# Optimization experiments

Measured on AMD Instinct MI355X. Metric: run time of the kernel, lower is better.

Reference implementation:

```python
import jax, jax.numpy as jnp
import numpy as np

D_MODEL = 1024
NUM_HEADS = 16
HEAD_DIM = D_MODEL // NUM_HEADS
CAUSAL = True


def rope_cos_sin(seq_len, dim):
    inv_freq = 1.0 / (10000.0 ** (jnp.arange(0, dim, 2, dtype=jnp.float32) / dim))
    t = jnp.arange(seq_len, dtype=jnp.float32)
    freqs = jnp.einsum('i,j->ij', t, inv_freq)          # [S, dim/2]
    emb = jnp.concatenate([freqs, freqs], axis=-1)      # [S, dim]
    return jnp.cos(emb), jnp.sin(emb)


def rotate_half(x):
    x1, x2 = jnp.split(x, 2, axis=-1)
    return jnp.concatenate([-x2, x1], axis=-1)


def setup_inputs() -> dict:
    key = jax.random.key(0)
    k1, k2, k3, k4, k5 = jax.random.split(key, 5)
    B, S = 2, 2048
    x = jax.random.normal(k1, (B, S, D_MODEL), dtype=jnp.float32)
    s = 1.0 / np.sqrt(D_MODEL)
    W_qkv = jax.random.normal(k2, (D_MODEL, 3 * D_MODEL), dtype=jnp.float32) * s
    b_qkv = jax.random.normal(k3, (3 * D_MODEL,), dtype=jnp.float32) * 0.01
    W_out = jax.random.normal(k4, (D_MODEL, D_MODEL), dtype=jnp.float32) * s
    b_out = jax.random.normal(k5, (D_MODEL,), dtype=jnp.float32) * 0.01
    return {"x": x, "W_qkv": W_qkv, "b_qkv": b_qkv, "W_out": W_out, "b_out": b_out}


def reference(x, W_qkv, b_qkv, W_out, b_out):
    B, S, _ = x.shape
    qkv = x @ W_qkv + b_qkv                              # [B, S, 3D]
    q, k, v = jnp.split(qkv, 3, axis=-1)
    # [B, H, S, hd]
    q = q.reshape(B, S, NUM_HEADS, HEAD_DIM).transpose(0, 2, 1, 3)
    k = k.reshape(B, S, NUM_HEADS, HEAD_DIM).transpose(0, 2, 1, 3)
    v = v.reshape(B, S, NUM_HEADS, HEAD_DIM).transpose(0, 2, 1, 3)
    cos, sin = rope_cos_sin(S, HEAD_DIM)                 # [S, hd]
    cos = cos[None, None]
    sin = sin[None, None]
    q = q * cos + rotate_half(q) * sin
    k = k * cos + rotate_half(k) * sin
    scores = jnp.einsum('bhqd,bhkd->bhqk', q, k) / np.sqrt(HEAD_DIM)
    if CAUSAL:
        causal_mask = jnp.triu(jnp.ones((S, S), dtype=bool), k=1)
        scores = jnp.where(causal_mask, -jnp.inf, scores)
    attn = jax.nn.softmax(scores, axis=-1)
    out = jnp.einsum('bhqk,bhkd->bhqd', attn, v)         # [B, H, S, hd]
    out = out.transpose(0, 2, 1, 3).reshape(B, S, D_MODEL)
    return out @ W_out + b_out
```

## Files before the change

### kernel.cpp

```cpp
#include <hip/hip_runtime.h>
#include <hip/hip_bf16.h>
#include <math.h>

typedef __bf16 bf16;
typedef __bf16 bf16x8 __attribute__((ext_vector_type(8)));
typedef unsigned short ushort8 __attribute__((ext_vector_type(8)));
typedef float floatx4 __attribute__((ext_vector_type(4)));

#define MFMA_BF16(a, b, c) __builtin_amdgcn_mfma_f32_16x16x32_bf16(a, b, c, 0, 0, 0)

__device__ __forceinline__ bf16x8 cvt8(const float4 a, const float4 b) {
  bf16x8 t;
  t[0] = (bf16)a.x; t[1] = (bf16)a.y; t[2] = (bf16)a.z; t[3] = (bf16)a.w;
  t[4] = (bf16)b.x; t[5] = (bf16)b.y; t[6] = (bf16)b.z; t[7] = (bf16)b.w;
  return t;
}

__device__ __forceinline__ unsigned int pack2(float a, float b) {
  unsigned short lo = __builtin_bit_cast(unsigned short, (bf16)a);
  unsigned short hi = __builtin_bit_cast(unsigned short, (bf16)b);
  return (unsigned int)lo | ((unsigned int)hi << 16);
}

__device__ __forceinline__ void gld16(const bf16* g, bf16* l) {
  __builtin_amdgcn_global_load_lds(
      (const __attribute__((address_space(1))) unsigned int*)g,
      (__attribute__((address_space(3))) unsigned int*)l, 16, 0, 0);
}

__global__ __launch_bounds__(256) void cast_x_kernel(const float* __restrict__ in,
                                                     bf16* __restrict__ out) {
  const int i = blockIdx.x * 256 + threadIdx.x;
  const float4 a = *(const float4*)&in[(size_t)i * 8];
  const float4 b = *(const float4*)&in[(size_t)i * 8 + 4];
  *(bf16x8*)&out[(size_t)i * 8] = cvt8(a, b);
}

__global__ __launch_bounds__(256) void transpose_w_kernel(
    const float* __restrict__ in, bf16* __restrict__ out, int N, int K) {
  __shared__ __align__(16) bf16 T[64][40];
  const int t = threadIdx.x;
  const int k0 = blockIdx.y * 32, n0 = blockIdx.x * 64;
  {
    const int k = t >> 3, n8 = (t & 7) * 8;
    const float* p = &in[(size_t)(k0 + k) * N + n0 + n8];
    const float4 a = *(const float4*)p;
    const float4 b = *(const float4*)(p + 4);
    const float v[8] = {a.x, a.y, a.z, a.w, b.x, b.y, b.z, b.w};
#pragma unroll
    for (int j = 0; j < 8; j++) {
      const int n = n8 + j;
      T[n][k ^ (8 * ((n >> 3) & 3))] = (bf16)v[j];
    }
  }
  __syncthreads();
  {
    const int n = t >> 2, k8 = (t & 3) * 8;
    const int kp = k8 ^ (8 * ((n >> 3) & 3));
    *(bf16x8*)&out[(size_t)(n0 + n) * K + k0 + k8] = *(const bf16x8*)&T[n][kp];
  }
}

template <int MODE>
__global__ __launch_bounds__(256) void gemm128_kernel(
    const bf16* __restrict__ A, const bf16* __restrict__ Bt,
    const float* __restrict__ bias, void* __restrict__ out0,
    bf16* __restrict__ outK, bf16* __restrict__ outV, int M, int N, int K) {
  __shared__ __align__(16) bf16 As[128][32];
  __shared__ __align__(16) bf16 Bs[128][32];

  const int tid = threadIdx.x, lane = tid & 63, w = tid >> 6;
  const int c = lane & 15, quad = lane >> 4;
  const int wm = w >> 1, wn = w & 1;
  const int m0 = blockIdx.y * 128, n0 = blockIdx.x * 128;
  const int srow = lane >> 2, scol = (lane & 3) * 8;

  floatx4 acc[4][4] = {};

  for (int k0 = 0; k0 < K; k0 += 32) {
    __syncthreads();
#pragma unroll
    for (int i = 0; i < 2; i++) {
      const int r = w * 32 + i * 16;
      gld16(&A[(size_t)(m0 + r + srow) * K + k0 + scol], &As[r][0]);
      gld16(&Bt[(size_t)(n0 + r + srow) * K + k0 + scol], &Bs[r][0]);
    }
    __syncthreads();

    bf16x8 af[4], bfr[4];
#pragma unroll
    for (int mi = 0; mi < 4; mi++)
      af[mi] = *(const bf16x8*)&As[wm * 64 + mi * 16 + c][quad * 8];
#pragma unroll
    for (int ni = 0; ni < 4; ni++)
      bfr[ni] = *(const bf16x8*)&Bs[wn * 64 + ni * 16 + c][quad * 8];

#pragma unroll
    for (int mi = 0; mi < 4; mi++)
#pragma unroll
      for (int ni = 0; ni < 4; ni++)
        acc[mi][ni] = MFMA_BF16(af[mi], bfr[ni], acc[mi][ni]);
  }

#pragma unroll
  for (int mi = 0; mi < 4; mi++) {
#pragma unroll
    for (int ni = 0; ni < 4; ni++) {
#pragma unroll
      for (int r = 0; r < 4; r++) {
        const int row = m0 + wm * 64 + mi * 16 + quad * 4 + r;
        const int col = n0 + wn * 64 + ni * 16 + c;
        const float v = acc[mi][ni][r] + bias[col];
        if (MODE == 0) {
          ((float*)out0)[(size_t)row * N + col] = v;
        } else {
          const int t = col >> 10;
          const int h = (col & 1023) >> 6;
          const int d = col & 63;
          const int b = row >> 11, s = row & 2047;
          bf16* dst = (t == 0) ? (bf16*)out0 : (t == 1 ? outK : outV);
          dst[(((size_t)b * 16 + h) * 2048 + s) * 64 + d] = (bf16)v;
        }
      }
    }
  }
}

__global__ __launch_bounds__(256) void rope_kernel(bf16* __restrict__ Q,
                                                   bf16* __restrict__ Kt) {
  const int idx = blockIdx.x * 256 + threadIdx.x;
  const int d = idx & 31;
  const int h = (idx >> 5) & 15;
  const int s = (idx >> 9) & 2047;
  const int b = idx >> 20;
  const size_t base = (((size_t)b * 16 + h) * 2048 + s) * 64 + d;

  const float inv = exp2f(-0.41524101186092f * (float)d);
  const float ang = (float)s * inv;
  float sn, cs;
  sincosf(ang, &sn, &cs);

  const float q1 = (float)Q[base], q2 = (float)Q[base + 32];
  const float k1 = (float)Kt[base], k2 = (float)Kt[base + 32];
  Q[base]       = (bf16)((q1 * cs - q2 * sn) * 0.125f);
  Q[base + 32]  = (bf16)((q2 * cs + q1 * sn) * 0.125f);
  Kt[base]      = (bf16)(k1 * cs - k2 * sn);
  Kt[base + 32] = (bf16)(k2 * cs + k1 * sn);
}

struct AttnState {
  floatx4 o[4];
  float l;
};

__device__ __forceinline__ void attn_step(
    const bf16x8 qf[2], const bf16x8 kf[4][2], const bf16x8 vf[4][2],
    bf16 (*PsW)[72], AttnState& st, int qglob, int kbase, bool diag, int c,
    int quad) {
  floatx4 sacc[4] = {};
#pragma unroll
  for (int kg = 0; kg < 4; kg++)
#pragma unroll
    for (int dh = 0; dh < 2; dh++)
      sacc[kg] = MFMA_BF16(kf[kg][dh], qf[dh], sacc[kg]);

#pragma unroll
  for (int kg = 0; kg < 4; kg++) {
    float p[4];
#pragma unroll
    for (int r = 0; r < 4; r++) {
      float e = __expf(sacc[kg][r]);
      if (diag && (kbase + kg * 16 + quad * 4 + r > qglob)) e = 0.0f;
      p[r] = e;
    }
    st.l += (p[0] + p[1]) + (p[2] + p[3]);
    const uint2 u = {pack2(p[0], p[1]), pack2(p[2], p[3])};
    *(uint2*)&PsW[c][kg * 16 + quad * 4] = u;
  }

  bf16x8 pf[2];
#pragma unroll
  for (int ks = 0; ks < 2; ks++)
    pf[ks] = *(const bf16x8*)&PsW[c][ks * 32 + quad * 8];

#pragma unroll
  for (int dg = 0; dg < 4; dg++)
#pragma unroll
    for (int ks = 0; ks < 2; ks++)
      st.o[dg] = MFMA_BF16(vf[dg][ks], pf[ks], st.o[dg]);
}

__global__ __launch_bounds__(256) void attn_kernel(const bf16* __restrict__ Q,
                                                   const bf16* __restrict__ K,
                                                   const bf16* __restrict__ V,
                                                   bf16* __restrict__ Aout) {
  const int S = 2048;
  const int bh = blockIdx.y;
  const int p = blockIdx.x;
  const int tid = threadIdx.x, lane = tid & 63, wave = tid >> 6;
  const int c = lane & 15, quad = lane >> 4;

  __shared__ __align__(16) bf16 Ks[64][72];
  __shared__ __align__(16) bf16 Vt[64][72];
  __shared__ __align__(16) bf16 Ps[4][16][72];

  const bf16* Qb = Q + (size_t)bh * S * 64;
  const bf16* Kb = K + (size_t)bh * S * 64;
  const bf16* Vb = V + (size_t)bh * S * 64;
  const int b = bh >> 4, h = bh & 15;

  const int qA = p, qB = 31 - p;
  const int qgA = qA * 64 + wave * 16 + c;
  const int qgB = qB * 64 + wave * 16 + c;

  bf16x8 qfA[2], qfB[2];
#pragma unroll
  for (int dh = 0; dh < 2; dh++) {
    qfA[dh] = *(const bf16x8*)&Qb[(size_t)qgA * 64 + dh * 32 + quad * 8];
    qfB[dh] = *(const bf16x8*)&Qb[(size_t)qgB * 64 + dh * 32 + quad * 8];
  }

  AttnState stA = {}, stB = {};

  const int vcc = (tid & 7) * 8;
  const int vr2 = ((tid >> 3) + 4 * (tid & 7)) & 31;

  for (int kt = 0; kt <= qB; kt++) {
    __syncthreads();
#pragma unroll
    for (int i = 0; i < 2; i++) {
      const int idx = tid + i * 256;
      const int r = idx >> 3, cc8 = (idx & 7) * 8;
      *(uint4*)&Ks[r][cc8] = *(const uint4*)&Kb[(size_t)(kt * 64 + r) * 64 + cc8];
    }
    {
      const bf16* vs = &Vb[(size_t)(kt * 64 + 2 * vr2) * 64 + vcc];
      const ushort8 w0 = __builtin_bit_cast(ushort8, *(const bf16x8*)vs);
      const ushort8 w1 = __builtin_bit_cast(ushort8, *(const bf16x8*)(vs + 64));
#pragma unroll
      for (int j = 0; j < 8; j++)
        *(unsigned int*)&Vt[vcc + j][2 * vr2] =
            (unsigned int)w0[j] | ((unsigned int)w1[j] << 16);
    }
    __syncthreads();

    bf16x8 kf[4][2];
#pragma unroll
    for (int kg = 0; kg < 4; kg++)
#pragma unroll
      for (int dh = 0; dh < 2; dh++)
        kf[kg][dh] = *(const bf16x8*)&Ks[kg * 16 + c][dh * 32 + quad * 8];

    bf16x8 vf[4][2];
#pragma unroll
    for (int dg = 0; dg < 4; dg++)
#pragma unroll
      for (int ks = 0; ks < 2; ks++)
        vf[dg][ks] = *(const bf16x8*)&Vt[dg * 16 + c][ks * 32 + quad * 8];

    attn_step(qfB, kf, vf, Ps[wave], stB, qgB, kt * 64, kt == qB, c, quad);
    if (kt <= qA)
      attn_step(qfA, kf, vf, Ps[wave], stA, qgA, kt * 64, kt == qA, c, quad);
  }

  stA.l += __shfl_xor(stA.l, 16);
  stA.l += __shfl_xor(stA.l, 32);
  stB.l += __shfl_xor(stB.l, 16);
  stB.l += __shfl_xor(stB.l, 32);
  const float ivA = 1.0f / stA.l, ivB = 1.0f / stB.l;

#pragma unroll
  for (int dg = 0; dg < 4; dg++) {
    const uint2 uA = {pack2(stA.o[dg][0] * ivA, stA.o[dg][1] * ivA),
                      pack2(stA.o[dg][2] * ivA, stA.o[dg][3] * ivA)};
    const uint2 uB = {pack2(stB.o[dg][0] * ivB, stB.o[dg][1] * ivB),
                      pack2(stB.o[dg][2] * ivB, stB.o[dg][3] * ivB)};
    *(uint2*)&Aout[((size_t)b * 2048 + qgA) * 1024 + h * 64 + dg * 16 + quad * 4] = uA;
    *(uint2*)&Aout[((size_t)b * 2048 + qgB) * 1024 + h * 64 + dg * 16 + quad * 4] = uB;
  }
}

extern "C" void kernel_launch(void* const* d_in, const int* in_sizes, int n_in,
                              void* d_out, int out_size, void* d_ws,
                              size_t ws_size, hipStream_t stream) {
  const float* x = (const float*)d_in[0];
  const float* W_qkv = (const float*)d_in[1];
  const float* b_qkv = (const float*)d_in[2];
  const float* W_out = (const float*)d_in[3];
  const float* b_out = (const float*)d_in[4];
  float* out = (float*)d_out;

  const int B = 2, S = 2048, NH = 16;
  const size_t qn = (size_t)B * NH * S * 64;

  bf16* xb = (bf16*)d_ws;
  bf16* Wqkvt = xb + qn;
  bf16* Wot = Wqkvt + 3072 * 1024;
  bf16* Qw = Wot + 1024 * 1024;
  bf16* Kw = Qw + qn;
  bf16* Vw = Kw + qn;
  bf16* AO = xb;

  cast_x_kernel<<<dim3(qn / 8 / 256), 256, 0, stream>>>(x, xb);
  transpose_w_kernel<<<dim3(3072 / 64, 1024 / 32), 256, 0, stream>>>(
      W_qkv, Wqkvt, 3072, 1024);
  transpose_w_kernel<<<dim3(1024 / 64, 1024 / 32), 256, 0, stream>>>(
      W_out, Wot, 1024, 1024);

  gemm128_kernel<1><<<dim3(3072 / 128, 4096 / 128), 256, 0, stream>>>(
      xb, Wqkvt, b_qkv, Qw, Kw, Vw, 4096, 3072, 1024);
  rope_kernel<<<dim3((B * S * NH * 32) / 256), 256, 0, stream>>>(Qw, Kw);
  attn_kernel<<<dim3(16, B * NH), 256, 0, stream>>>(Qw, Kw, Vw, AO);
  gemm128_kernel<0><<<dim3(1024 / 128, 4096 / 128), 256, 0, stream>>>(
      AO, Wot, b_out, out, nullptr, nullptr, 4096, 1024, 1024);
}
```

Baseline: 218.4 us.

## Deepen GEMM K-step to 64, use narrower out-proj tile, async K loads in attention

The GEMM now stages 64-wide K slices as two 32-wide halves per barrier pair, which halves the number of syncthreads per K loop. It is templated on the N tile, and the output projection uses a 64-wide N tile so the grid has twice as many blocks and fills the device better. The attention kernel now loads K tiles with the gld16 direct-to-LDS path into a split [2][64][32] layout instead of register-staged uint4 copies. The trade-off is more LDS per GEMM block, which may lower occupancy.

Result: faster. 205.9 us (-5.7%).

```diff
diff --git a/kernel.cpp b/kernel.cpp
--- a/kernel.cpp
+++ b/kernel.cpp
@@ -61,55 +61,67 @@
   }
 }
 
-template <int MODE>
-__global__ __launch_bounds__(256) void gemm128_kernel(
+template <int TN, int MODE>
+__global__ __launch_bounds__(256) void gemm_kernel(
     const bf16* __restrict__ A, const bf16* __restrict__ Bt,
     const float* __restrict__ bias, void* __restrict__ out0,
     bf16* __restrict__ outK, bf16* __restrict__ outV, int M, int N, int K) {
-  __shared__ __align__(16) bf16 As[128][32];
-  __shared__ __align__(16) bf16 Bs[128][32];
+  constexpr int NI = TN / 32;
+  constexpr int BI = TN / 32;
+  __shared__ __align__(16) bf16 As2[2][128][32];
+  __shared__ __align__(16) bf16 Bs2[2][TN][32];
 
   const int tid = threadIdx.x, lane = tid & 63, w = tid >> 6;
   const int c = lane & 15, quad = lane >> 4;
   const int wm = w >> 1, wn = w & 1;
-  const int m0 = blockIdx.y * 128, n0 = blockIdx.x * 128;
+  const int m0 = blockIdx.y * 128, n0 = blockIdx.x * TN;
   const int srow = lane >> 2, scol = (lane & 3) * 8;
 
-  floatx4 acc[4][4] = {};
-
-  for (int k0 = 0; k0 < K; k0 += 32) {
+  floatx4 acc[4][NI] = {};
+
+  for (int k0 = 0; k0 < K; k0 += 64) {
     __syncthreads();
 #pragma unroll
-    for (int i = 0; i < 2; i++) {
-      const int r = w * 32 + i * 16;
-      gld16(&A[(size_t)(m0 + r + srow) * K + k0 + scol], &As[r][0]);
-      gld16(&Bt[(size_t)(n0 + r + srow) * K + k0 + scol], &Bs[r][0]);
+    for (int i = 0; i < 4; i++) {
+      const int seg = w * 4 + i;
+      const int kh = seg >> 3, r0 = (seg & 7) * 16;
+      gld16(&A[(size_t)(m0 + r0 + srow) * K + k0 + kh * 32 + scol],
+            &As2[kh][r0][0]);
+    }
+#pragma unroll
+    for (int i = 0; i < BI; i++) {
+      const int seg = w * BI + i;
+      const int kh = seg / (TN / 16), r0 = (seg % (TN / 16)) * 16;
+      gld16(&Bt[(size_t)(n0 + r0 + srow) * K + k0 + kh * 32 + scol],
+            &Bs2[kh][r0][0]);
     }
     __syncthreads();
 
-    bf16x8 af[4], bfr[4];
-#pragma unroll
-    for (int mi = 0; mi < 4; mi++)
-      af[mi] = *(const bf16x8*)&As[wm * 64 + mi * 16 + c][quad * 8];
-#pragma unroll
-    for (int ni = 0; ni < 4; ni++)
-      bfr[ni] = *(const bf16x8*)&Bs[wn * 64 + ni * 16 + c][quad * 8];
-
-#pragma unroll
-    for (int mi = 0; mi < 4; mi++)
-#pragma unroll
-      for (int ni = 0; ni < 4; ni++)
-        acc[mi][ni] = MFMA_BF16(af[mi], bfr[ni], acc[mi][ni]);
+#pragma unroll
+    for (int kh = 0; kh < 2; kh++) {
+      bf16x8 af[4], bfr[NI];
+#pragma unroll
+      for (int mi = 0; mi < 4; mi++)
+        af[mi] = *(const bf16x8*)&As2[kh][wm * 64 + mi * 16 + c][quad * 8];
+#pragma unroll
+      for (int ni = 0; ni < NI; ni++)
+        bfr[ni] = *(const bf16x8*)&Bs2[kh][wn * (TN / 2) + ni * 16 + c][quad * 8];
+#pragma unroll
+      for (int mi = 0; mi < 4; mi++)
+#pragma unroll
+        for (int ni = 0; ni < NI; ni++)
+          acc[mi][ni] = MFMA_BF16(af[mi], bfr[ni], acc[mi][ni]);
+    }
   }
 
 #pragma unroll
   for (int mi = 0; mi < 4; mi++) {
 #pragma unroll
-    for (int ni = 0; ni < 4; ni++) {
+    for (int ni = 0; ni < NI; ni++) {
 #pragma unroll
       for (int r = 0; r < 4; r++) {
         const int row = m0 + wm * 64 + mi * 16 + quad * 4 + r;
-        const int col = n0 + wn * 64 + ni * 16 + c;
+        const int col = n0 + wn * (TN / 2) + ni * 16 + c;
         const float v = acc[mi][ni][r] + bias[col];
         if (MODE == 0) {
           ((float*)out0)[(size_t)row * N + col] = v;
@@ -200,7 +212,7 @@
   const int tid = threadIdx.x, lane = tid & 63, wave = tid >> 6;
   const int c = lane & 15, quad = lane >> 4;
 
-  __shared__ __align__(16) bf16 Ks[64][72];
+  __shared__ __align__(16) bf16 Ks2[2][64][32];
   __shared__ __align__(16) bf16 Vt[64][72];
   __shared__ __align__(16) bf16 Ps[4][16][72];
 
@@ -224,14 +236,16 @@
 
   const int vcc = (tid & 7) * 8;
   const int vr2 = ((tid >> 3) + 4 * (tid & 7)) & 31;
+  const int ksr = lane >> 2, ksc = (lane & 3) * 8;
 
   for (int kt = 0; kt <= qB; kt++) {
     __syncthreads();
 #pragma unroll
     for (int i = 0; i < 2; i++) {
-      const int idx = tid + i * 256;
-      const int r = idx >> 3, cc8 = (idx & 7) * 8;
-      *(uint4*)&Ks[r][cc8] = *(const uint4*)&Kb[(size_t)(kt * 64 + r) * 64 + cc8];
+      const int seg = wave * 2 + i;
+      const int dh = seg >> 2, r0 = (seg & 3) * 16;
+      gld16(&Kb[(size_t)(kt * 64 + r0 + ksr) * 64 + dh * 32 + ksc],
+            &Ks2[dh][r0][0]);
     }
     {
       const bf16* vs = &Vb[(size_t)(kt * 64 + 2 * vr2) * 64 + vcc];
@@ -249,7 +263,7 @@
     for (int kg = 0; kg < 4; kg++)
 #pragma unroll
       for (int dh = 0; dh < 2; dh++)
-        kf[kg][dh] = *(const bf16x8*)&Ks[kg * 16 + c][dh * 32 + quad * 8];
+        kf[kg][dh] = *(const bf16x8*)&Ks2[dh][kg * 16 + c][quad * 8];
 
     bf16x8 vf[4][2];
 #pragma unroll
@@ -307,10 +321,10 @@
   transpose_w_kernel<<<dim3(1024 / 64, 1024 / 32), 256, 0, stream>>>(
       W_out, Wot, 1024, 1024);
 
-  gemm128_kernel<1><<<dim3(3072 / 128, 4096 / 128), 256, 0, stream>>>(
+  gemm_kernel<128, 1><<<dim3(3072 / 128, 4096 / 128), 256, 0, stream>>>(
       xb, Wqkvt, b_qkv, Qw, Kw, Vw, 4096, 3072, 1024);
   rope_kernel<<<dim3((B * S * NH * 32) / 256), 256, 0, stream>>>(Qw, Kw);
   attn_kernel<<<dim3(16, B * NH), 256, 0, stream>>>(Qw, Kw, Vw, AO);
-  gemm128_kernel<0><<<dim3(1024 / 128, 4096 / 128), 256, 0, stream>>>(
+  gemm_kernel<64, 0><<<dim3(1024 / 64, 4096 / 128), 256, 0, stream>>>(
       AO, Wot, b_out, out, nullptr, nullptr, 4096, 1024, 1024);
 }
```
